# Optimization experiments

Measured on AMD Instinct MI355X. Metric: run time of the kernel, lower is better.

The kernel has to match this reference:

```python
import jax, jax.numpy as jnp
import numpy as np

H = 32  # hidden_size
T = 7   # num_day (seq_len)
F = 1   # num_feature
B = 262144


def _glorot(key, shape):
    # mimic torch uniform(-1/sqrt(H), 1/sqrt(H)) init for LSTM/Linear params
    bound = 1.0 / np.sqrt(H)
    return jax.random.uniform(key, shape, jnp.float32, -bound, bound)


def setup_inputs() -> dict:
    key = jax.random.key(0)
    ks = jax.random.split(key, 14)
    return {
        "inputs": jax.random.normal(ks[0], (B, T, F), jnp.float32),
        # layer 0 (input_size=F)
        "W_ih0": _glorot(ks[1], (4 * H, F)),
        "W_hh0": _glorot(ks[2], (4 * H, H)),
        "b_ih0": _glorot(ks[3], (4 * H,)),
        "b_hh0": _glorot(ks[4], (4 * H,)),
        # layer 1 (input_size=H)
        "W_ih1": _glorot(ks[5], (4 * H, H)),
        "W_hh1": _glorot(ks[6], (4 * H, H)),
        "b_ih1": _glorot(ks[7], (4 * H,)),
        "b_hh1": _glorot(ks[8], (4 * H,)),
        # fc: Linear(H, 1)
        "fc_w": _glorot(ks[9], (1, H)),
        "fc_b": _glorot(ks[10], (1,)),
        # fc1: Linear(T, 1)
        "fc1_w": jax.random.uniform(ks[11], (1, T), jnp.float32, -1.0 / np.sqrt(T), 1.0 / np.sqrt(T)),
        "fc1_b": jax.random.uniform(ks[12], (1,), jnp.float32, -1.0 / np.sqrt(T), 1.0 / np.sqrt(T)),
    }


def _lstm_layer(x_tbf, W_ih, W_hh, b):
    # x_tbf: [T, B, in]; PyTorch gate order: i, f, g, o
    Bdim = x_tbf.shape[1]
    h0 = jnp.zeros((Bdim, H), x_tbf.dtype)
    c0 = jnp.zeros((Bdim, H), x_tbf.dtype)

    def step(carry, x_t):
        h, c = carry
        gates = x_t @ W_ih.T + h @ W_hh.T + b  # [B, 4H]
        i, f, g, o = jnp.split(gates, 4, axis=-1)
        i = jax.nn.sigmoid(i)
        f = jax.nn.sigmoid(f)
        g = jnp.tanh(g)
        o = jax.nn.sigmoid(o)
        c = f * c + i * g
        h = o * jnp.tanh(c)
        return (h, c), h

    _, hs = jax.lax.scan(step, (h0, c0), x_tbf)
    return hs  # [T, B, H]


def reference(inputs, W_ih0, W_hh0, b_ih0, b_hh0, W_ih1, W_hh1, b_ih1, b_hh1,
              fc_w, fc_b, fc1_w, fc1_b):
    x = jnp.transpose(inputs, (1, 0, 2))            # [T, B, F]
    h1 = _lstm_layer(x, W_ih0, W_hh0, b_ih0 + b_hh0)  # [T, B, H]
    h2 = _lstm_layer(h1, W_ih1, W_hh1, b_ih1 + b_hh1)  # [T, B, H]
    out = jnp.transpose(h2, (1, 0, 2))              # [B, T, H]
    y = out @ fc_w.T + fc_b                          # [B, T, 1]
    y = jnp.squeeze(y, 2)                            # [B, T]
    y = y @ fc1_w.T + fc1_b                          # [B, 1]
    return y
```

## Files before the change

kernel.cpp:

```cpp
#include <hip/hip_runtime.h>


#define HID 32
#define TSTEPS 7
#define LSTRIDE 36
#define NWAVES 4

typedef _Float16 half8 __attribute__((ext_vector_type(8)));
typedef float floatx4 __attribute__((ext_vector_type(4)));
typedef float floatx2 __attribute__((ext_vector_type(2)));

#define LOG2E 1.44269504088896f

__device__ __forceinline__ float fast_rcp(float x) { return __builtin_amdgcn_rcpf(x); }

__device__ __forceinline__ float exp2_fast(float x) {
#if __has_builtin(__builtin_amdgcn_exp2f)
    return __builtin_amdgcn_exp2f(x);
#else
    return __expf(x * 0.69314718055994531f);
#endif
}

__device__ __forceinline__ floatx2 mk2(float a, float b) {
    floatx2 v; v[0] = a; v[1] = b; return v;
}
__device__ __forceinline__ floatx2 exp2_v2(floatx2 a) {
    return mk2(exp2_fast(a[0]), exp2_fast(a[1]));
}

__device__ __forceinline__ floatx2 cell_pair(floatx2 gi, floatx2 gf,
                                             floatx2 gg, floatx2 go,
                                             floatx2& cst) {
    const floatx2 one = mk2(1.0f, 1.0f);
    const floatx2 Ea = exp2_v2(gi);
    const floatx2 Db = exp2_v2(gf) + one;
    const floatx2 Ed = exp2_v2(gg);
    const floatx2 Ee = exp2_v2(go);
    const floatx2 M  = (Ea + one) * (Ed + one);
    const float Rb = fast_rcp(Db[0] * Db[1]);
    const float Rm = fast_rcp(M[0] * M[1]);
    const floatx2 ff  = mk2(Rb, Rb) * mk2(Db[1], Db[0]);
    const floatx2 rig = mk2(Rm, Rm) * mk2(M[1], M[0]);
    const floatx2 ig  = __builtin_elementwise_fma(Ed, rig, -rig);
    const floatx2 c   = __builtin_elementwise_fma(ff, cst, ig);
    cst = c;
    const floatx2 Ec  = exp2_v2(c * mk2(2.0f * LOG2E, 2.0f * LOG2E));
    const floatx2 Dh  = (Ee + one) * (Ec + one);
    const float Rh = fast_rcp(Dh[0] * Dh[1]);
    const floatx2 th = mk2(Rh, Rh) * mk2(Dh[1], Dh[0]);
    return __builtin_elementwise_fma(Ec, th, -th);
}

__global__ __launch_bounds__(256, 2) void lstm2_mfma(
    const float* __restrict__ xin,
    const float* __restrict__ Wih0,
    const float* __restrict__ Whh0,
    const float* __restrict__ bih0,
    const float* __restrict__ bhh0,
    const float* __restrict__ Wih1,
    const float* __restrict__ Whh1,
    const float* __restrict__ bih1,
    const float* __restrict__ bhh1,
    const float* __restrict__ fcw,
    const float* __restrict__ fcb,
    const float* __restrict__ fc1w,
    const float* __restrict__ fc1b,
    float* __restrict__ out,
    int B)
{
    const int lane = threadIdx.x & 63;
    const int wave = threadIdx.x >> 6;
    const int col  = lane & 15;
    const int rg   = lane >> 4;
    const int seq_base = (blockIdx.x * NWAVES + wave) * 16;

    __shared__ __align__(16) _Float16 ldsw[3 * 8 * 64 * 8];
    __shared__ __align__(16) floatx2  ldsbw0[128];
    __shared__ float                  ldsb1[128];
    __shared__ __align__(16) _Float16 ldsh[NWAVES][16 * LSTRIDE];
    __shared__ __align__(16) float    ldsx[NWAVES][TSTEPS * 16];

    _Float16* hl = &ldsh[wave][0];
    float* xl = &ldsx[wave][0];

#pragma unroll
    for (int e = lane; e < TSTEPS * 16; e += 64) {
        const int s = e / TSTEPS;
        const int tt = e - s * TSTEPS;
        xl[tt * 16 + s] = xin[seq_base * TSTEPS + e];
    }

    if (wave < 3) {
        const float* Wsrc = (wave == 0) ? Whh0 : (wave == 1) ? Wih1 : Whh1;
#pragma unroll
        for (int nt = 0; nt < 8; ++nt) {
            const int n = nt * 16 + col;
            const float sc = ((n >> 5) == 2) ? (2.0f * LOG2E) : (-LOG2E);
            const float* s = Wsrc + n * HID + rg * 8;
            half8 f;
#pragma unroll
            for (int j = 0; j < 8; ++j) f[j] = (_Float16)(sc * s[j]);
            *(half8*)&ldsw[((wave * 8 + nt) * 64 + lane) * 8] = f;
        }
    } else {
#pragma unroll
        for (int i = 0; i < 2; ++i) {
            const int n = i * 64 + lane;
            const float sc = ((n >> 5) == 2) ? (2.0f * LOG2E) : (-LOG2E);
            floatx2 bw;
            bw[0] = sc * (bih0[n] + bhh0[n]);
            bw[1] = sc * Wih0[n];
            ldsbw0[n] = bw;
            ldsb1[n]  = sc * (bih1[n] + bhh1[n]);
        }
    }
    __syncthreads();

    const float fcw_l0 = fcw[col];
    const float fcw_l1 = fcw[16 + col];

    half8 Ah1 = {};
    half8 Ah2 = {};
    floatx2 c1v[2][2] = {}, c2v[2][2] = {};
    floatx2 faccv[2] = {};

    for (int t = 0; t < TSTEPS; ++t) {
        unsigned woff = 0;
        asm volatile("" : "+v"(woff));
        const char* wB  = (const char*)ldsw   + lane * 16 + woff;
        const char* bB0 = (const char*)ldsbw0 + col * 8  + woff;
        const char* bB1 = (const char*)ldsb1  + col * 4  + woff;

        const floatx4 xr = *(const floatx4*)&xl[t * 16 + rg * 4];

        floatx4 g0[8];
#pragma unroll
        for (int nt = 0; nt < 8; ++nt) {
            const floatx2 bw = *(const floatx2*)(bB0 + nt * 128);
            const half8 bf   = *(const half8*)(wB + nt * 1024);
            const floatx2 wv = mk2(bw[1], bw[1]);
            const floatx2 bv = mk2(bw[0], bw[0]);
            const floatx2 clo = __builtin_elementwise_fma(wv, mk2(xr[0], xr[1]), bv);
            const floatx2 chi = __builtin_elementwise_fma(wv, mk2(xr[2], xr[3]), bv);
            floatx4 c;
            c[0] = clo[0]; c[1] = clo[1]; c[2] = chi[0]; c[3] = chi[1];
            g0[nt] = __builtin_amdgcn_mfma_f32_16x16x32_f16(Ah1, bf, c, 0, 0, 0);
        }

#pragma unroll
        for (int q = 0; q < 2; ++q) {
#pragma unroll
            for (int rp = 0; rp < 2; ++rp) {
                const floatx2 h = cell_pair(
                    mk2(g0[0 + q][rp * 2], g0[0 + q][rp * 2 + 1]),
                    mk2(g0[2 + q][rp * 2], g0[2 + q][rp * 2 + 1]),
                    mk2(g0[4 + q][rp * 2], g0[4 + q][rp * 2 + 1]),
                    mk2(g0[6 + q][rp * 2], g0[6 + q][rp * 2 + 1]),
                    c1v[q][rp]);
                hl[(rg * 4 + rp * 2 + 0) * LSTRIDE + q * 16 + col] = (_Float16)h[0];
                hl[(rg * 4 + rp * 2 + 1) * LSTRIDE + q * 16 + col] = (_Float16)h[1];
            }
        }
        Ah1 = *(const half8*)&hl[col * LSTRIDE + rg * 8];

        floatx4 g1[8];
#pragma unroll
        for (int nt = 0; nt < 8; ++nt) {
            const float b1  = *(const float*)(bB1 + nt * 64);
            const half8 f1a = *(const half8*)(wB + 8192  + nt * 1024);
            const half8 f1b = *(const half8*)(wB + 16384 + nt * 1024);
            floatx4 c = {b1, b1, b1, b1};
            c = __builtin_amdgcn_mfma_f32_16x16x32_f16(Ah1, f1a, c, 0, 0, 0);
            g1[nt] = __builtin_amdgcn_mfma_f32_16x16x32_f16(Ah2, f1b, c, 0, 0, 0);
        }

        const float f1t = fc1w[t];
        const float w0 = f1t * fcw_l0;
        const float w1 = f1t * fcw_l1;
#pragma unroll
        for (int q = 0; q < 2; ++q) {
            const float wq = q ? w1 : w0;
            const floatx2 wqv = mk2(wq, wq);
#pragma unroll
            for (int rp = 0; rp < 2; ++rp) {
                const floatx2 h = cell_pair(
                    mk2(g1[0 + q][rp * 2], g1[0 + q][rp * 2 + 1]),
                    mk2(g1[2 + q][rp * 2], g1[2 + q][rp * 2 + 1]),
                    mk2(g1[4 + q][rp * 2], g1[4 + q][rp * 2 + 1]),
                    mk2(g1[6 + q][rp * 2], g1[6 + q][rp * 2 + 1]),
                    c2v[q][rp]);
                faccv[rp] = __builtin_elementwise_fma(wqv, h, faccv[rp]);
                hl[(rg * 4 + rp * 2 + 0) * LSTRIDE + q * 16 + col] = (_Float16)h[0];
                hl[(rg * 4 + rp * 2 + 1) * LSTRIDE + q * 16 + col] = (_Float16)h[1];
            }
        }
        Ah2 = *(const half8*)&hl[col * LSTRIDE + rg * 8];
    }

    float facc[4];
#pragma unroll
    for (int r = 0; r < 4; ++r) facc[r] = faccv[r >> 1][r & 1];
#pragma unroll
    for (int r = 0; r < 4; ++r) {
        float v = facc[r];
        v += __shfl_xor(v, 1);
        v += __shfl_xor(v, 2);
        v += __shfl_xor(v, 4);
        v += __shfl_xor(v, 8);
        facc[r] = v;
    }
    float sum_f1 = 0.f;
#pragma unroll
    for (int t = 0; t < TSTEPS; ++t) sum_f1 += fc1w[t];
    const float tail = fcb[0] * sum_f1 + fc1b[0];

    if (col == 0) {
#pragma unroll
        for (int r = 0; r < 4; ++r)
            out[seq_base + rg * 4 + r] = facc[r] + tail;
    }
}

extern "C" void kernel_launch(void* const* d_in, const int* in_sizes, int n_in,
                              void* d_out, int out_size, void* d_ws, size_t ws_size,
                              hipStream_t stream) {
    const float* xin  = (const float*)d_in[0];
    const float* Wih0 = (const float*)d_in[1];
    const float* Whh0 = (const float*)d_in[2];
    const float* bih0 = (const float*)d_in[3];
    const float* bhh0 = (const float*)d_in[4];
    const float* Wih1 = (const float*)d_in[5];
    const float* Whh1 = (const float*)d_in[6];
    const float* bih1 = (const float*)d_in[7];
    const float* bhh1 = (const float*)d_in[8];
    const float* fcw  = (const float*)d_in[9];
    const float* fcb  = (const float*)d_in[10];
    const float* fc1w = (const float*)d_in[11];
    const float* fc1b = (const float*)d_in[12];
    float* out = (float*)d_out;

    const int B = in_sizes[0] / TSTEPS;
    const int grid = B / (NWAVES * 16);
    lstm2_mfma<<<grid, NWAVES * 64, 0, stream>>>(
        xin, Wih0, Whh0, bih0, bhh0, Wih1, Whh1, bih1, bhh1,
        fcw, fcb, fc1w, fc1b, out, B);
}
```

Measured before the change: 190.6 us.

## Software-pipeline layer-0 gate MFMAs for next step into current iteration

Moves the layer-0 gate matrix multiplies for step t+1 so they are issued right after the layer-1 MFMAs of step t, using the freshly computed h1. At t=0 the gates reduce to the input term, so the MFMA with a zero hidden state is skipped. The aim is to let the layer-0 MFMAs of the next step overlap with the layer-1 cell math and hide MFMA latency along the dependency chain. In exchange, eight extra floatx4 accumulators stay live across iterations, which raises register pressure and may lower occupancy.

Result: no change. 191.1 us (+0.3%).

```diff
diff --git a/kernel.cpp b/kernel.cpp
--- a/kernel.cpp
+++ b/kernel.cpp
@@ -120,10 +120,21 @@
     const float fcw_l0 = fcw[col];
     const float fcw_l1 = fcw[16 + col];
 
-    half8 Ah1 = {};
     half8 Ah2 = {};
     floatx2 c1v[2][2] = {}, c2v[2][2] = {};
     floatx2 faccv[2] = {};
+
+    floatx4 g0c[8];
+    {
+        const floatx4 xr0 = *(const floatx4*)&xl[rg * 4];
+        const char* bB0p = (const char*)ldsbw0 + col * 8;
+#pragma unroll
+        for (int nt = 0; nt < 8; ++nt) {
+            const floatx2 bw = *(const floatx2*)(bB0p + nt * 128);
+#pragma unroll
+            for (int r = 0; r < 4; ++r) g0c[nt][r] = fmaf(bw[1], xr0[r], bw[0]);
+        }
+    }
 
     for (int t = 0; t < TSTEPS; ++t) {
         unsigned woff = 0;
@@ -132,37 +143,21 @@
         const char* bB0 = (const char*)ldsbw0 + col * 8  + woff;
         const char* bB1 = (const char*)ldsb1  + col * 4  + woff;
 
-        const floatx4 xr = *(const floatx4*)&xl[t * 16 + rg * 4];
-
-        floatx4 g0[8];
-#pragma unroll
-        for (int nt = 0; nt < 8; ++nt) {
-            const floatx2 bw = *(const floatx2*)(bB0 + nt * 128);
-            const half8 bf   = *(const half8*)(wB + nt * 1024);
-            const floatx2 wv = mk2(bw[1], bw[1]);
-            const floatx2 bv = mk2(bw[0], bw[0]);
-            const floatx2 clo = __builtin_elementwise_fma(wv, mk2(xr[0], xr[1]), bv);
-            const floatx2 chi = __builtin_elementwise_fma(wv, mk2(xr[2], xr[3]), bv);
-            floatx4 c;
-            c[0] = clo[0]; c[1] = clo[1]; c[2] = chi[0]; c[3] = chi[1];
-            g0[nt] = __builtin_amdgcn_mfma_f32_16x16x32_f16(Ah1, bf, c, 0, 0, 0);
-        }
-
 #pragma unroll
         for (int q = 0; q < 2; ++q) {
 #pragma unroll
             for (int rp = 0; rp < 2; ++rp) {
                 const floatx2 h = cell_pair(
-                    mk2(g0[0 + q][rp * 2], g0[0 + q][rp * 2 + 1]),
-                    mk2(g0[2 + q][rp * 2], g0[2 + q][rp * 2 + 1]),
-                    mk2(g0[4 + q][rp * 2], g0[4 + q][rp * 2 + 1]),
-                    mk2(g0[6 + q][rp * 2], g0[6 + q][rp * 2 + 1]),
+                    mk2(g0c[0 + q][rp * 2], g0c[0 + q][rp * 2 + 1]),
+                    mk2(g0c[2 + q][rp * 2], g0c[2 + q][rp * 2 + 1]),
+                    mk2(g0c[4 + q][rp * 2], g0c[4 + q][rp * 2 + 1]),
+                    mk2(g0c[6 + q][rp * 2], g0c[6 + q][rp * 2 + 1]),
                     c1v[q][rp]);
                 hl[(rg * 4 + rp * 2 + 0) * LSTRIDE + q * 16 + col] = (_Float16)h[0];
                 hl[(rg * 4 + rp * 2 + 1) * LSTRIDE + q * 16 + col] = (_Float16)h[1];
             }
         }
-        Ah1 = *(const half8*)&hl[col * LSTRIDE + rg * 8];
+        const half8 Ah1 = *(const half8*)&hl[col * LSTRIDE + rg * 8];
 
         floatx4 g1[8];
 #pragma unroll
@@ -173,6 +168,19 @@
             floatx4 c = {b1, b1, b1, b1};
             c = __builtin_amdgcn_mfma_f32_16x16x32_f16(Ah1, f1a, c, 0, 0, 0);
             g1[nt] = __builtin_amdgcn_mfma_f32_16x16x32_f16(Ah2, f1b, c, 0, 0, 0);
+        }
+
+        if (t + 1 < TSTEPS) {
+            const floatx4 xr = *(const floatx4*)&xl[(t + 1) * 16 + rg * 4];
+#pragma unroll
+            for (int nt = 0; nt < 8; ++nt) {
+                const floatx2 bw = *(const floatx2*)(bB0 + nt * 128);
+                const half8 bf   = *(const half8*)(wB + nt * 1024);
+                floatx4 c;
+#pragma unroll
+                for (int r = 0; r < 4; ++r) c[r] = fmaf(bw[1], xr[r], bw[0]);
+                g0c[nt] = __builtin_amdgcn_mfma_f32_16x16x32_f16(Ah1, bf, c, 0, 0, 0);
+            }
         }
 
         const float f1t = fc1w[t];
```
